# Optimization experiments

Measured on AMD Instinct MI355X. Metric: run time of the kernel, lower is better.

The kernel has to match this reference:

```python
import jax, jax.numpy as jnp
import numpy as np

B, S, D, K = 2, 4096, 512, 32
EPS = 1e-8


def _cantor_measure(n, levels=24):
    """Devil's staircase (Cantor function) evaluated at i/(n-1)."""
    t = np.arange(n, dtype=np.float64) / max(n - 1, 1)
    c = np.zeros(n)
    r = t.copy()
    done = np.zeros(n, dtype=bool)
    scale = 0.5
    for _ in range(levels):
        r = r * 3.0
        d = np.clip(np.floor(r).astype(np.int64), 0, 2)
        r = r - d
        add = np.where(d == 2, scale, 0.0) + np.where(d == 1, scale, 0.0)
        c = np.where(done, c, c + add)
        done = done | (d == 1)
        scale *= 0.5
    return c


def _build_routes_and_weights(n, k):
    """Cantor-distance k-nearest routing (seq_len, k) and normalized fusion weights."""
    c = _cantor_measure(n)
    dist = np.abs(c[:, None] - c[None, :])  # (S, S), built once on host
    idx = np.argsort(dist, axis=1, kind='stable')[:, :k].astype(np.int32)
    d = np.take_along_axis(dist, idx, axis=1)
    w = np.exp(-d)  # geometric 'weighted' fusion mode
    w = w / (w.sum(axis=1, keepdims=True) + EPS)
    return idx, w.astype(np.float32)


def setup_inputs() -> dict:
    key = jax.random.key(0)
    k1, k2, k3, k4 = jax.random.split(key, 4)
    routes_np, weights_np = _build_routes_and_weights(S, K)
    return {
        'x': jax.random.normal(k1, (B, S, D), dtype=jnp.float32),
        'W_in': jax.random.normal(k2, (D, D), dtype=jnp.float32) * (1.0 / np.sqrt(D)),
        'W_out': jax.random.normal(k3, (D, D), dtype=jnp.float32) * (1.0 / np.sqrt(D)),
        'b_out': jax.random.normal(k4, (D,), dtype=jnp.float32) * 0.02,
        'fusion_weights': jnp.asarray(weights_np),
        'routes': jnp.asarray(routes_np),
    }


def reference(x, W_in, W_out, b_out, fusion_weights, routes):
    # 1. input projection (bias-free), heads are a contiguous split of D so
    #    the shared per-position weights make the per-head fuse equal to a flat fuse
    h = x @ W_in                                  # (B, S, D)
    # 2. gather fusion window per position (irregular Cantor routing)
    g = jnp.take(h, routes, axis=1)               # (B, S, K, D)
    # 3. weighted fusion with normalized staircase-distance weights
    fused = jnp.einsum('bskd,sk->bsd', g, fusion_weights)
    # 4. output projection + residual
    out = fused @ W_out + b_out
    return x + out
```

## Files before the change

### kernel.cpp

```cpp
#include <hip/hip_runtime.h>
#include <hip/hip_bf16.h>
#include <stdint.h>

#define S_LEN  4096
#define D_DIM  512
#define K_R    32
#define M_ROWS 8192

typedef __attribute__((ext_vector_type(8))) short bf16x8;
typedef __attribute__((ext_vector_type(4))) float f32x4;

__device__ __forceinline__ float bf2f(short u) {
  union { unsigned int i; float f; } c;
  c.i = ((unsigned int)(unsigned short)u) << 16;
  return c.f;
}

__device__ __forceinline__ void gload_lds16(const void* g, void* lds) {
  __builtin_amdgcn_global_load_lds(
      (__attribute__((address_space(1))) void*)g,
      (__attribute__((address_space(3))) void*)lds, 16, 0, 0);
}

__device__ __forceinline__ int4 pack8(float4 v0, float4 v1) {
  union { __hip_bfloat16 h[8]; int4 v; } u;
  u.h[0] = __float2bfloat16(v0.x); u.h[1] = __float2bfloat16(v0.y);
  u.h[2] = __float2bfloat16(v0.z); u.h[3] = __float2bfloat16(v0.w);
  u.h[4] = __float2bfloat16(v1.x); u.h[5] = __float2bfloat16(v1.y);
  u.h[6] = __float2bfloat16(v1.z); u.h[7] = __float2bfloat16(v1.w);
  return u.v;
}

__global__ void __launch_bounds__(256) prep_kernel(
    const float* __restrict__ x, __hip_bfloat16* __restrict__ xb,
    const float* __restrict__ Win, __hip_bfloat16* __restrict__ Winb,
    const float* __restrict__ Wout, __hip_bfloat16* __restrict__ WoutTb) {
  __shared__ __hip_bfloat16 Lds[64][66];
  const int tid = threadIdx.x;
  if (blockIdx.x < 2048) {
    const int i = blockIdx.x * 256 + tid;
    const float4* xp = (const float4*)x;
    ((int4*)xb)[i] = pack8(xp[2 * i], xp[2 * i + 1]);
    return;
  }
  if (blockIdx.x < 2112) {
    const int e4 = ((blockIdx.x - 2048) * 256 + tid) * 4;
    const float4* wp = (const float4*)Win;
    int4* op = (int4*)Winb;
#pragma unroll
    for (int h = 0; h < 2; ++h)
      op[e4 / 2 + h] = pack8(wp[e4 + 2 * h], wp[e4 + 2 * h + 1]);
    return;
  }
  const int bx = blockIdx.x - 2112;
  const int tr = (bx >> 3) * 64;
  const int tc = (bx & 7) * 64;
#pragma unroll
  for (int it = 0; it < 4; ++it) {
    const int id = it * 256 + tid;
    const int r = id >> 4, c4 = (id & 15) * 4;
    const float4 v = *(const float4*)&Wout[(size_t)(tr + r) * 512 + tc + c4];
    Lds[r][c4]     = __float2bfloat16(v.x);
    Lds[r][c4 + 1] = __float2bfloat16(v.y);
    Lds[r][c4 + 2] = __float2bfloat16(v.z);
    Lds[r][c4 + 3] = __float2bfloat16(v.w);
  }
  __syncthreads();
#pragma unroll
  for (int it = 0; it < 2; ++it) {
    const int id = it * 256 + tid;
    const int j = id >> 3, i0 = (id & 7) * 8;
    union { __hip_bfloat16 h[8]; int4 v; } u;
#pragma unroll
    for (int r = 0; r < 8; ++r) u.h[r] = Lds[i0 + r][j];
    *(int4*)&WoutTb[(size_t)(tc + j) * 512 + tr + i0] = u.v;
  }
}

#define BM 128
#define BN 64
#define BK 64

__global__ void __launch_bounds__(256) mid_kernel(
    const __hip_bfloat16* __restrict__ xb,
    const float* __restrict__ fw,
    const int* __restrict__ routes,
    __hip_bfloat16* __restrict__ g,
    const __hip_bfloat16* __restrict__ WoutTb,
    const __hip_bfloat16* __restrict__ Winb,
    __hip_bfloat16* __restrict__ WcT) {
  __shared__ __hip_bfloat16 As[BM][BK];
  __shared__ __hip_bfloat16 Bs[BN][BK];
  __shared__ float w_s[4][K_R];
  __shared__ int   r_s[4][K_R];
  const int tid = threadIdx.x;
  const int w = tid >> 6, l = tid & 63;

  if (blockIdx.x >= 32) {
    const int lin = blockIdx.x - 32;
    const int bchunk = (lin & 7) * 256 + (lin >> 3);
    const int row = bchunk * 4 + w;
    const int s = row & (S_LEN - 1);
    const int b = row >> 12;
    if (l < K_R) {
      r_s[w][l] = routes[s * K_R + l];
      w_s[w][l] = fw[s * K_R + l];
    }
    __syncthreads();
    const __hip_bfloat16* xbb = xb + (size_t)b * S_LEN * D_DIM + l * 8;
    float acc[8] = {};
#pragma unroll 8
    for (int k = 0; k < K_R; ++k) {
      const float wk = w_s[w][k];
      const bf16x8 v = *(const bf16x8*)(xbb + (size_t)r_s[w][k] * D_DIM);
#pragma unroll
      for (int j = 0; j < 8; ++j) acc[j] = fmaf(wk, bf2f(v[j]), acc[j]);
    }
    union { __hip_bfloat16 h[8]; int4 v; } u;
#pragma unroll
    for (int j = 0; j < 8; ++j) u.h[j] = __float2bfloat16(acc[j]);
    *(int4*)(g + (size_t)row * D_DIM + l * 8) = u.v;
    return;
  }

  const int id2 = blockIdx.x;
  const int bm0 = (id2 >> 3) * BM;
  const int bn0 = (id2 & 7) * BN;
  const int wr  = (w >> 1) * 64;
  const int wcn = (w & 1) * 32;

  const int rin = l >> 3;
  const int usw = (l & 7) ^ rin;
  const __hip_bfloat16* gA = WoutTb + (size_t)(bm0 + w * 8 + rin) * D_DIM + usw * 8;
  const __hip_bfloat16* gB = Winb   + (size_t)(bn0 + w * 8 + rin) * D_DIM + usw * 8;
  __hip_bfloat16* ldsA = &As[w * 8][0];
  __hip_bfloat16* ldsB = &Bs[w * 8][0];
  const int fr = l & 15, fq = l >> 4;

  f32x4 acc[4][2] = {};
  for (int k0 = 0; k0 < D_DIM; k0 += BK) {
#pragma unroll
    for (int i = 0; i < 4; ++i)
      gload_lds16(gA + (size_t)(i * 32) * D_DIM + k0, ldsA + i * 32 * BK);
#pragma unroll
    for (int j = 0; j < 2; ++j)
      gload_lds16(gB + (size_t)(j * 32) * D_DIM + k0, ldsB + j * 32 * BK);
    __syncthreads();
#pragma unroll
    for (int kk = 0; kk < 2; ++kk) {
      const int u = (kk * 4 + fq) ^ (fr & 7);
      bf16x8 af[4], bfv[2];
#pragma unroll
      for (int m = 0; m < 4; ++m)
        af[m] = *(const bf16x8*)&As[wr + m * 16 + fr][u * 8];
#pragma unroll
      for (int n = 0; n < 2; ++n)
        bfv[n] = *(const bf16x8*)&Bs[wcn + n * 16 + fr][u * 8];
#pragma unroll
      for (int m = 0; m < 4; ++m)
#pragma unroll
        for (int n = 0; n < 2; ++n)
          acc[m][n] = __builtin_amdgcn_mfma_f32_16x16x32_bf16(af[m], bfv[n], acc[m][n], 0, 0, 0);
    }
    __syncthreads();
  }
#pragma unroll
  for (int m = 0; m < 4; ++m)
#pragma unroll
    for (int n = 0; n < 2; ++n)
#pragma unroll
      for (int r = 0; r < 4; ++r) {
        const int grow = bm0 + wr + m * 16 + fq * 4 + r;
        const int gcol = bn0 + wcn + n * 16 + fr;
        WcT[(size_t)grow * D_DIM + gcol] = __float2bfloat16(acc[m][n][r]);
      }
}

#define GBN 128

__global__ void __launch_bounds__(512, 4) gemm_out_kernel(
    const __hip_bfloat16* __restrict__ A,
    const __hip_bfloat16* __restrict__ BT,
    const float* __restrict__ x,
    const float* __restrict__ b_out,
    float* __restrict__ out) {
  __shared__ __hip_bfloat16 As[2][BM][BK];
  __shared__ __hip_bfloat16 Bs[2][GBN][BK];
  const int tid = threadIdx.x;
  const int w = tid >> 6, l = tid & 63;

  const int bid = blockIdx.x;
  const int id2 = (bid & 7) * 32 + (bid >> 3);
  const int bm0 = (id2 >> 2) * BM;
  const int bn0 = (id2 & 3) * GBN;

  const int wr  = (w >> 2) * 64;
  const int wcn = (w & 3) * 32;

  const int rin = l >> 3;
  const int usw = (l & 7) ^ rin;
  const __hip_bfloat16* gA = A + (size_t)(bm0 + w * 16 + rin) * D_DIM + usw * 8;
  const __hip_bfloat16* gB = BT + (size_t)(bn0 + w * 16 + rin) * D_DIM + usw * 8;

  const int fr = l & 15, fq = l >> 4;
  f32x4 acc[4][2] = {};

#define STAGE(buf, k0)                                                          \
  {                                                                             \
    _Pragma("unroll")                                                           \
    for (int i = 0; i < 2; ++i)                                                 \
      gload_lds16(gA + (size_t)(i * 8) * D_DIM + (k0),                          \
                  &As[buf][w * 16 + i * 8][0]);                                 \
    _Pragma("unroll")                                                           \
    for (int j = 0; j < 2; ++j)                                                 \
      gload_lds16(gB + (size_t)(j * 8) * D_DIM + (k0),                          \
                  &Bs[buf][w * 16 + j * 8][0]);                                 \
  }

#define COMPUTE(buf)                                                            \
  {                                                                             \
    _Pragma("unroll")                                                           \
    for (int kk = 0; kk < 2; ++kk) {                                            \
      const int u = (kk * 4 + fq) ^ (fr & 7);                                   \
      bf16x8 af[4], bfv[2];                                                     \
      _Pragma("unroll")                                                         \
      for (int m = 0; m < 4; ++m)                                               \
        af[m] = *(const bf16x8*)&As[buf][wr + m * 16 + fr][u * 8];              \
      _Pragma("unroll")                                                         \
      for (int n = 0; n < 2; ++n)                                               \
        bfv[n] = *(const bf16x8*)&Bs[buf][wcn + n * 16 + fr][u * 8];            \
      _Pragma("unroll")                                                         \
      for (int m = 0; m < 4; ++m)                                               \
        _Pragma("unroll")                                                       \
        for (int n = 0; n < 2; ++n)                                             \
          acc[m][n] = __builtin_amdgcn_mfma_f32_16x16x32_bf16(                  \
              af[m], bfv[n], acc[m][n], 0, 0, 0);                               \
    }                                                                           \
  }

  STAGE(0, 0);
#pragma unroll
  for (int t = 0; t < 7; ++t) {
    STAGE((t + 1) & 1, (t + 1) * BK);
    asm volatile("s_waitcnt vmcnt(4)" ::: "memory");
    __builtin_amdgcn_s_barrier();
    __builtin_amdgcn_sched_barrier(0);
    COMPUTE(t & 1);
    __builtin_amdgcn_s_barrier();
  }
  asm volatile("s_waitcnt vmcnt(0)" ::: "memory");
  __builtin_amdgcn_s_barrier();
  __builtin_amdgcn_sched_barrier(0);
  COMPUTE(1);
#undef STAGE
#undef COMPUTE

  const float bb0 = b_out[bn0 + wcn + fr];
  const float bb1 = b_out[bn0 + wcn + 16 + fr];
#pragma unroll
  for (int m = 0; m < 4; ++m)
#pragma unroll
    for (int r = 0; r < 4; ++r) {
      const int grow = bm0 + wr + m * 16 + fq * 4 + r;
      const size_t base = (size_t)grow * D_DIM + bn0 + wcn + fr;
      out[base]      = acc[m][0][r] + x[base]      + bb0;
      out[base + 16] = acc[m][1][r] + x[base + 16] + bb1;
    }
}

extern "C" void kernel_launch(void* const* d_in, const int* in_sizes, int n_in,
                              void* d_out, int out_size, void* d_ws, size_t ws_size,
                              hipStream_t stream) {
  const float* x      = (const float*)d_in[0];
  const float* W_in   = (const float*)d_in[1];
  const float* W_out  = (const float*)d_in[2];
  const float* b_out  = (const float*)d_in[3];
  const float* fw     = (const float*)d_in[4];
  const int*   routes = (const int*)d_in[5];
  float* out = (float*)d_out;

  char* ws = (char*)d_ws;
  __hip_bfloat16* Xb     = (__hip_bfloat16*)ws;
  __hip_bfloat16* WcT    = (__hip_bfloat16*)(ws + 8388608);
  __hip_bfloat16* g      = (__hip_bfloat16*)(ws + 8912896);
  __hip_bfloat16* Winb   = (__hip_bfloat16*)(ws + 17301504);
  __hip_bfloat16* WoutTb = (__hip_bfloat16*)(ws + 17825792);

  prep_kernel<<<2176, 256, 0, stream>>>(x, Xb, W_in, Winb, W_out, WoutTb);
  mid_kernel<<<2080, 256, 0, stream>>>(Xb, fw, routes, g, WoutTb, Winb, WcT);
  gemm_out_kernel<<<256, 512, 0, stream>>>(g, WcT, x, b_out, out);
}
```

Measured before the change: 35.38 us.

## Stage contiguous route window of X rows in LDS for gather-fuse blocks

Each gather block now handles 16 output rows instead of 4. It finds the min and max route index over those rows with LDS atomics and, when the span fits in 48 rows, bulk-loads that window of Xb into shared memory with global_load_lds so the 32-way weighted gather reads from LDS. Otherwise it falls back to the direct global gather. This aims to cut redundant global or L2 reads of the same neighbour rows, since Cantor routes are locally clustered. It costs more LDS per block (about 48KB, lowering occupancy), extra barriers and atomics, and fewer blocks in the grid.

```diff
diff --git a/kernel.cpp b/kernel.cpp
--- a/kernel.cpp
+++ b/kernel.cpp
@@ -80,6 +80,13 @@
 #define BM 128
 #define BN 64
 #define BK 64
+#define WCAP 48
+
+union MidSMem {
+  struct { __hip_bfloat16 As[BM][BK]; __hip_bfloat16 Bs[BN][BK]; } wc;
+  struct { ushort X[WCAP * 512]; int r[16][32]; float w[16][32];
+           int lo, hi; } ga;
+};
 
 __global__ void __launch_bounds__(256) mid_kernel(
     const __hip_bfloat16* __restrict__ xb,
@@ -89,37 +96,71 @@
     const __hip_bfloat16* __restrict__ WoutTb,
     const __hip_bfloat16* __restrict__ Winb,
     __hip_bfloat16* __restrict__ WcT) {
-  __shared__ __hip_bfloat16 As[BM][BK];
-  __shared__ __hip_bfloat16 Bs[BN][BK];
-  __shared__ float w_s[4][K_R];
-  __shared__ int   r_s[4][K_R];
+  __shared__ MidSMem sm;
   const int tid = threadIdx.x;
   const int w = tid >> 6, l = tid & 63;
 
   if (blockIdx.x >= 32) {
     const int lin = blockIdx.x - 32;
-    const int bchunk = (lin & 7) * 256 + (lin >> 3);
-    const int row = bchunk * 4 + w;
-    const int s = row & (S_LEN - 1);
-    const int b = row >> 12;
-    if (l < K_R) {
-      r_s[w][l] = routes[s * K_R + l];
-      w_s[w][l] = fw[s * K_R + l];
-    }
-    __syncthreads();
-    const __hip_bfloat16* xbb = xb + (size_t)b * S_LEN * D_DIM + l * 8;
-    float acc[8] = {};
+    const int bchunk = (lin & 7) * 64 + (lin >> 3);
+    const int r0 = bchunk * 16;
+    const int s0 = r0 & (S_LEN - 1);
+    const int b = r0 >> 12;
+    if (tid == 0) { sm.ga.lo = 0x7fffffff; sm.ga.hi = 0; }
+    __syncthreads();
+#pragma unroll
+    for (int it = 0; it < 2; ++it) {
+      const int idx = it * 256 + tid;
+      const int rl = idx >> 5, k = idx & 31;
+      const int rt = routes[(s0 + rl) * K_R + k];
+      sm.ga.r[rl][k] = rt;
+      sm.ga.w[rl][k] = fw[(s0 + rl) * K_R + k];
+      atomicMin(&sm.ga.lo, rt);
+      atomicMax(&sm.ga.hi, rt);
+    }
+    __syncthreads();
+    const int lo = min(sm.ga.lo, S_LEN - WCAP);
+    const bool staged = (sm.ga.hi - lo) < WCAP;
+    const __hip_bfloat16* xbat = xb + (size_t)b * S_LEN * D_DIM;
+    if (staged) {
+#pragma unroll
+      for (int it = 0; it < 12; ++it) {
+        const int row = lo + it * 4 + (tid >> 6);
+        gload_lds16(xbat + (size_t)row * D_DIM + l * 8,
+                    sm.ga.X + it * 2048 + w * 512);
+      }
+    }
+    __syncthreads();
+
+#pragma unroll
+    for (int rr = 0; rr < 4; ++rr) {
+      const int rl = w * 4 + rr;
+      const int row = r0 + rl;
+      float acc[8] = {};
+      if (staged) {
 #pragma unroll 8
-    for (int k = 0; k < K_R; ++k) {
-      const float wk = w_s[w][k];
-      const bf16x8 v = *(const bf16x8*)(xbb + (size_t)r_s[w][k] * D_DIM);
-#pragma unroll
-      for (int j = 0; j < 8; ++j) acc[j] = fmaf(wk, bf2f(v[j]), acc[j]);
-    }
-    union { __hip_bfloat16 h[8]; int4 v; } u;
-#pragma unroll
-    for (int j = 0; j < 8; ++j) u.h[j] = __float2bfloat16(acc[j]);
-    *(int4*)(g + (size_t)row * D_DIM + l * 8) = u.v;
+        for (int k = 0; k < K_R; ++k) {
+          const float wk = sm.ga.w[rl][k];
+          const int rt = sm.ga.r[rl][k] - lo;
+          const bf16x8 v = *(const bf16x8*)(sm.ga.X + rt * 512 + l * 8);
+#pragma unroll
+          for (int j = 0; j < 8; ++j) acc[j] = fmaf(wk, bf2f(v[j]), acc[j]);
+        }
+      } else {
+#pragma unroll 8
+        for (int k = 0; k < K_R; ++k) {
+          const float wk = sm.ga.w[rl][k];
+          const bf16x8 v =
+              *(const bf16x8*)(xbat + (size_t)sm.ga.r[rl][k] * D_DIM + l * 8);
+#pragma unroll
+          for (int j = 0; j < 8; ++j) acc[j] = fmaf(wk, bf2f(v[j]), acc[j]);
+        }
+      }
+      union { __hip_bfloat16 h[8]; int4 v; } u;
+#pragma unroll
+      for (int j = 0; j < 8; ++j) u.h[j] = __float2bfloat16(acc[j]);
+      *(int4*)(g + (size_t)row * D_DIM + l * 8) = u.v;
+    }
     return;
   }
 
@@ -133,8 +174,8 @@
   const int usw = (l & 7) ^ rin;
   const __hip_bfloat16* gA = WoutTb + (size_t)(bm0 + w * 8 + rin) * D_DIM + usw * 8;
   const __hip_bfloat16* gB = Winb   + (size_t)(bn0 + w * 8 + rin) * D_DIM + usw * 8;
-  __hip_bfloat16* ldsA = &As[w * 8][0];
-  __hip_bfloat16* ldsB = &Bs[w * 8][0];
+  __hip_bfloat16* ldsA = &sm.wc.As[w * 8][0];
+  __hip_bfloat16* ldsB = &sm.wc.Bs[w * 8][0];
   const int fr = l & 15, fq = l >> 4;
 
   f32x4 acc[4][2] = {};
@@ -152,10 +193,10 @@
       bf16x8 af[4], bfv[2];
 #pragma unroll
       for (int m = 0; m < 4; ++m)
-        af[m] = *(const bf16x8*)&As[wr + m * 16 + fr][u * 8];
+        af[m] = *(const bf16x8*)&sm.wc.As[wr + m * 16 + fr][u * 8];
 #pragma unroll
       for (int n = 0; n < 2; ++n)
-        bfv[n] = *(const bf16x8*)&Bs[wcn + n * 16 + fr][u * 8];
+        bfv[n] = *(const bf16x8*)&sm.wc.Bs[wcn + n * 16 + fr][u * 8];
 #pragma unroll
       for (int m = 0; m < 4; ++m)
 #pragma unroll
@@ -287,6 +328,6 @@
   __hip_bfloat16* WoutTb = (__hip_bfloat16*)(ws + 17825792);
 
   prep_kernel<<<2176, 256, 0, stream>>>(x, Xb, W_in, Winb, W_out, WoutTb);
-  mid_kernel<<<2080, 256, 0, stream>>>(Xb, fw, routes, g, WoutTb, Winb, WcT);
+  mid_kernel<<<544, 256, 0, stream>>>(Xb, fw, routes, g, WoutTb, Winb, WcT);
   gemm_out_kernel<<<256, 512, 0, stream>>>(g, WcT, x, b_out, out);
 }
```

After: 50.72 us. 43.3% more time.
